# Performance work log

Hardware: AMD Instinct MI355X
Metric: run time of the kernel (lower is better)

## Reference

```python
import jax, jax.numpy as jnp
import numpy as np

N = 5_000_000   # total nodes
B = 16384       # number of graphs
F_X = 4
F_U = 1


def setup_inputs() -> dict:
    key = jax.random.key(0)
    k = jax.random.split(key, 6)
    x = jax.random.normal(k[0], (N, F_X), dtype=jnp.float32)
    batch = jnp.sort(jax.random.randint(k[1], (N,), 0, B)).astype(jnp.int64)
    u = jax.random.normal(k[2], (B, F_U), dtype=jnp.float32)
    d = F_U + F_X  # 5
    W1 = jax.random.normal(k[3], (d, d), dtype=jnp.float32) / np.sqrt(d)
    b1 = jnp.zeros((d,), dtype=jnp.float32)
    W2 = jax.random.normal(k[4], (d, F_U), dtype=jnp.float32) / np.sqrt(d)
    b2 = jnp.zeros((F_U,), dtype=jnp.float32)
    return {"x": x, "batch": batch, "u": u, "W1": W1, "b1": b1, "W2": W2, "b2": b2}


def reference(x, batch, u, W1, b1, W2, b2):
    # scatter_mean(x, batch, dim=0): segment sum / segment count (empty -> 0)
    seg_sum = jax.ops.segment_sum(x, batch, num_segments=B)            # [B, F_x]
    cnt = jax.ops.segment_sum(jnp.ones((x.shape[0],), x.dtype), batch,
                              num_segments=B)                          # [B]
    mean = jnp.where(cnt[:, None] > 0, seg_sum / jnp.maximum(cnt, 1.0)[:, None], 0.0)
    h = jnp.concatenate([u, mean], axis=1)                             # [B, 5]
    h = jax.nn.leaky_relu(h @ W1 + b1, negative_slope=0.1)
    return h @ W2 + b2                                                 # [B, 1]
```

## Files before the change

kernel.cpp:

```cpp
#include <hip/hip_runtime.h>

#define WAVE 64

typedef float v4f __attribute__((ext_vector_type(4)));
typedef int   v4i __attribute__((ext_vector_type(4)));

__global__ void find_starts4_kernel(const int* __restrict__ batch,
                                    int* __restrict__ seg_start,
                                    int N, int B) {
    const int tid  = blockIdx.x * blockDim.x + threadIdx.x;
    const int lane = threadIdx.x & (WAVE - 1);
    const long long i0 = (long long)tid * 4;
    const bool in   = (i0 < N);
    const bool full = (i0 + 3 < N);

    v4i q = (v4i)(0);
    if (full) q = __builtin_nontemporal_load(&((const v4i*)batch)[tid]);

    int prevw = __shfl_up(q.w, 1);

    if (!in) return;

    int prev;
    if (lane == 0) prev = (i0 == 0) ? -1 : batch[i0 - 1];
    else           prev = prevw;

    if (full) {
        int e[4] = {q.x, q.y, q.z, q.w};
        #pragma unroll
        for (int k = 0; k < 4; ++k) {
            int cur = e[k];
            for (int s = prev + 1; s <= cur; ++s) seg_start[s] = (int)(i0 + k);
            prev = cur;
        }
    } else {
        for (long long j = i0; j < N; ++j) {
            int cur = batch[j];
            for (int s = prev + 1; s <= cur; ++s) seg_start[s] = (int)j;
            prev = cur;
        }
    }

    if (i0 + 4 >= N) {
        for (int s = prev + 1; s <= B; ++s) seg_start[s] = N;
    }
}

__global__ void __launch_bounds__(256)
seg_mean_mlp_kernel(const v4f* __restrict__ x,
                    const int* __restrict__ seg_start,
                    const float* __restrict__ u,
                    const float* __restrict__ W1,
                    const float* __restrict__ b1,
                    const float* __restrict__ W2,
                    const float* __restrict__ b2,
                    float* __restrict__ out, int B) {
    const int wid  = (blockIdx.x * blockDim.x + threadIdx.x) >> 6;
    const int lane = threadIdx.x & (WAVE - 1);
    if (wid >= B) return;

    const int start = seg_start[wid];
    const int end   = seg_start[wid + 1];

    v4f a0 = (v4f)(0.f);
    v4f a1 = (v4f)(0.f);
    v4f a2 = (v4f)(0.f);
    v4f a3 = (v4f)(0.f);

    int i = start + lane;
    for (; i + 3 * WAVE < end; i += 4 * WAVE) {
        v4f v0 = __builtin_nontemporal_load(&x[i]);
        v4f v1 = __builtin_nontemporal_load(&x[i + WAVE]);
        v4f v2 = __builtin_nontemporal_load(&x[i + 2 * WAVE]);
        v4f v3 = __builtin_nontemporal_load(&x[i + 3 * WAVE]);
        a0 += v0; a1 += v1; a2 += v2; a3 += v3;
    }
    for (; i < end; i += WAVE) {
        v4f v = __builtin_nontemporal_load(&x[i]);
        a0 += v;
    }

    a0 += a1; a2 += a3; a0 += a2;

    float sx = a0.x, sy = a0.y, sz = a0.z, sw = a0.w;
    #pragma unroll
    for (int off = 32; off > 0; off >>= 1) {
        sx += __shfl_down(sx, off);
        sy += __shfl_down(sy, off);
        sz += __shfl_down(sz, off);
        sw += __shfl_down(sw, off);
    }

    if (lane == 0) {
        const int cnt = end - start;
        const float inv = (cnt > 0) ? (1.0f / (float)cnt) : 0.0f;

        float h[5];
        h[0] = u[wid];
        h[1] = sx * inv;
        h[2] = sy * inv;
        h[3] = sz * inv;
        h[4] = sw * inv;

        float o = b2[0];
        #pragma unroll
        for (int j = 0; j < 5; ++j) {
            float s = b1[j];
            #pragma unroll
            for (int i2 = 0; i2 < 5; ++i2) s += h[i2] * W1[i2 * 5 + j];
            s = (s > 0.0f) ? s : 0.1f * s;
            o += s * W2[j];
        }
        out[wid] = o;
    }
}

extern "C" void kernel_launch(void* const* d_in, const int* in_sizes, int n_in,
                              void* d_out, int out_size, void* d_ws, size_t ws_size,
                              hipStream_t stream) {
    const float* x     = (const float*)d_in[0];
    const int*   batch = (const int*)  d_in[1];
    const float* u     = (const float*)d_in[2];
    const float* W1    = (const float*)d_in[3];
    const float* b1    = (const float*)d_in[4];
    const float* W2    = (const float*)d_in[5];
    const float* b2    = (const float*)d_in[6];
    float* out = (float*)d_out;

    const int N = in_sizes[0] / 4;
    const int B = out_size;

    int* seg_start = (int*)d_ws;

    const int quads = (N + 3) / 4;
    find_starts4_kernel<<<(quads + 255) / 256, 256, 0, stream>>>(batch, seg_start, N, B);

    const int threads = 256;
    const int blocks  = (int)(((long long)B * WAVE + threads - 1) / threads);
    seg_mean_mlp_kernel<<<blocks, threads, 0, stream>>>(
        (const v4f*)x, seg_start, u, W1, b1, W2, b2, out, B);
}
```

Baseline: 140.7 us.

## Fuse segment-boundary search into mean+MLP kernel via per-wave parallel search

Drops the separate kernel that scanned the whole batch array to build segment starts. Instead, each wave locates its own segment's start and end with a 32-way parallel search over the sorted batch array, with each half-wave handling one boundary. The search window is guessed from a uniform-distribution estimate of ±8192 around t*N/B and falls back to the full range if the guess is wrong. This saves one kernel launch and a full 20MB pass over batch, at the cost of a few dependent global-memory search rounds per wave before accumulation can start.

```diff
diff --git a/kernel.cpp b/kernel.cpp
--- a/kernel.cpp
+++ b/kernel.cpp
@@ -3,64 +3,56 @@
 #define WAVE 64
 
 typedef float v4f __attribute__((ext_vector_type(4)));
-typedef int   v4i __attribute__((ext_vector_type(4)));
-
-__global__ void find_starts4_kernel(const int* __restrict__ batch,
-                                    int* __restrict__ seg_start,
-                                    int N, int B) {
-    const int tid  = blockIdx.x * blockDim.x + threadIdx.x;
-    const int lane = threadIdx.x & (WAVE - 1);
-    const long long i0 = (long long)tid * 4;
-    const bool in   = (i0 < N);
-    const bool full = (i0 + 3 < N);
-
-    v4i q = (v4i)(0);
-    if (full) q = __builtin_nontemporal_load(&((const v4i*)batch)[tid]);
-
-    int prevw = __shfl_up(q.w, 1);
-
-    if (!in) return;
-
-    int prev;
-    if (lane == 0) prev = (i0 == 0) ? -1 : batch[i0 - 1];
-    else           prev = prevw;
-
-    if (full) {
-        int e[4] = {q.x, q.y, q.z, q.w};
-        #pragma unroll
-        for (int k = 0; k < 4; ++k) {
-            int cur = e[k];
-            for (int s = prev + 1; s <= cur; ++s) seg_start[s] = (int)(i0 + k);
-            prev = cur;
-        }
-    } else {
-        for (long long j = i0; j < N; ++j) {
-            int cur = batch[j];
-            for (int s = prev + 1; s <= cur; ++s) seg_start[s] = (int)j;
-            prev = cur;
-        }
-    }
-
-    if (i0 + 4 >= N) {
-        for (int s = prev + 1; s <= B; ++s) seg_start[s] = N;
-    }
-}
 
 __global__ void __launch_bounds__(256)
-seg_mean_mlp_kernel(const v4f* __restrict__ x,
-                    const int* __restrict__ seg_start,
-                    const float* __restrict__ u,
-                    const float* __restrict__ W1,
-                    const float* __restrict__ b1,
-                    const float* __restrict__ W2,
-                    const float* __restrict__ b2,
-                    float* __restrict__ out, int B) {
+fused_seg_mean_mlp(const v4f* __restrict__ x,
+                   const int* __restrict__ batch,
+                   const float* __restrict__ u,
+                   const float* __restrict__ W1,
+                   const float* __restrict__ b1,
+                   const float* __restrict__ W2,
+                   const float* __restrict__ b2,
+                   float* __restrict__ out,
+                   int N, int B) {
     const int wid  = (blockIdx.x * blockDim.x + threadIdx.x) >> 6;
     const int lane = threadIdx.x & (WAVE - 1);
     if (wid >= B) return;
 
-    const int start = seg_start[wid];
-    const int end   = seg_start[wid + 1];
+    const int t   = wid + (lane >> 5);
+    const int sub = lane & 31;
+
+    const long long g = ((long long)t * (long long)N) / (long long)B;
+    int lo = (int)(g - 8192 > 0 ? g - 8192 : 0);
+    int hi = (int)(g + 8192 < (long long)N ? g + 8192 : (long long)N);
+
+    if (lo > 0 && batch[lo - 1] >= t) lo = 0;
+    if (hi < N && batch[hi] < t)      hi = N;
+
+    while (lo < hi) {
+        const int range = hi - lo;
+        const int s = (range + 31) >> 5;
+        const long long pi = (long long)lo + (long long)sub * (long long)s;
+        bool ge = true;
+        if (pi < (long long)hi) ge = (batch[pi] >= t);
+        const unsigned long long bal = __ballot(ge);
+        const unsigned grp = (lane >= 32) ? (unsigned)(bal >> 32)
+                                          : (unsigned)(bal & 0xffffffffu);
+        if (grp == 0u) {
+            const int nlo = lo + 31 * s + 1;
+            lo = (nlo < hi) ? nlo : hi;
+        } else {
+            const int f = __builtin_ctz(grp);
+            if (f == 0) {
+                hi = lo;
+            } else {
+                const int nhi = lo + f * s;
+                hi = (nhi < hi) ? nhi : hi;
+                lo = lo + (f - 1) * s + 1;
+            }
+        }
+    }
+    const int start = __shfl(lo, 0);
+    const int end   = __shfl(lo, 32);
 
     v4f a0 = (v4f)(0.f);
     v4f a1 = (v4f)(0.f);
@@ -76,8 +68,7 @@
         a0 += v0; a1 += v1; a2 += v2; a3 += v3;
     }
     for (; i < end; i += WAVE) {
-        v4f v = __builtin_nontemporal_load(&x[i]);
-        a0 += v;
+        a0 += __builtin_nontemporal_load(&x[i]);
     }
 
     a0 += a1; a2 += a3; a0 += a2;
@@ -105,11 +96,11 @@
         float o = b2[0];
         #pragma unroll
         for (int j = 0; j < 5; ++j) {
-            float s = b1[j];
+            float s2 = b1[j];
             #pragma unroll
-            for (int i2 = 0; i2 < 5; ++i2) s += h[i2] * W1[i2 * 5 + j];
-            s = (s > 0.0f) ? s : 0.1f * s;
-            o += s * W2[j];
+            for (int i2 = 0; i2 < 5; ++i2) s2 += h[i2] * W1[i2 * 5 + j];
+            s2 = (s2 > 0.0f) ? s2 : 0.1f * s2;
+            o += s2 * W2[j];
         }
         out[wid] = o;
     }
@@ -130,13 +121,10 @@
     const int N = in_sizes[0] / 4;
     const int B = out_size;
 
-    int* seg_start = (int*)d_ws;
-
-    const int quads = (N + 3) / 4;
-    find_starts4_kernel<<<(quads + 255) / 256, 256, 0, stream>>>(batch, seg_start, N, B);
+    (void)d_ws; (void)ws_size;
 
     const int threads = 256;
     const int blocks  = (int)(((long long)B * WAVE + threads - 1) / threads);
-    seg_mean_mlp_kernel<<<blocks, threads, 0, stream>>>(
-        (const v4f*)x, seg_start, u, W1, b1, W2, b2, out, B);
+    fused_seg_mean_mlp<<<blocks, threads, 0, stream>>>(
+        (const v4f*)x, batch, u, W1, b1, W2, b2, out, N, B);
 }
```

New measurement: 144.6 us. 1.03x slower.
